# Kernel tuning notes

Hardware: AMD Instinct MI355X
Metric: run time of the kernel (lower is better)

The kernel has to match this reference:

```python
import jax, jax.numpy as jnp
import numpy as np

NUM_HEADS = 12

def setup_inputs() -> dict:
    key = jax.random.key(0)
    k1, k2, k3 = jax.random.split(key, 3)
    B, N, C = 8, 2048, 768
    x = jax.random.normal(k1, (B, N, C), dtype=jnp.float32)
    w_qkv = jax.random.normal(k2, (3 * C, C), dtype=jnp.float32) * (C ** -0.5)
    w_proj = jax.random.normal(k3, (C, C), dtype=jnp.float32) * (C ** -0.5)
    b_proj = jnp.zeros((C,), dtype=jnp.float32)
    return {"x": x, "w_qkv": w_qkv, "w_proj": w_proj, "b_proj": b_proj}

def reference(x, w_qkv, w_proj, b_proj):
    B, N, C = x.shape
    H = NUM_HEADS
    D = C // H
    scale = D ** -0.5
    # qkv: [B,N,3C] -> [3,B,H,N,D]
    qkv = (x @ w_qkv.T).reshape(B, N, 3, H, D).transpose(2, 0, 3, 1, 4)
    q, k, v = qkv[0], qkv[1], qkv[2]
    attn = jnp.einsum('bhnd,bhmd->bhnm', q, k) * scale  # [B,H,N,N]
    attn = jax.nn.softmax(attn, axis=-1)
    out = jnp.einsum('bhnm,bhmd->bhnd', attn, v)  # [B,H,N,D]
    out = out.transpose(0, 2, 1, 3).reshape(B, N, C)
    return out @ w_proj.T + b_proj
```

## Files before the change

### kernel.cpp

```cpp
#include <hip/hip_runtime.h>

typedef __bf16 bf16;
typedef __attribute__((ext_vector_type(8))) __bf16 bf16x8;
typedef __attribute__((ext_vector_type(4))) __bf16 bf16x4;
typedef __attribute__((ext_vector_type(4))) float f32x4;

#define NBATCH 8
#define NHEAD  12
#define SEQ    2048
#define DH     64
#define CDIM   768
#define MROWS  (NBATCH*SEQ)
#define NQKV   (3*CDIM)

__device__ __forceinline__ f32x4 mfma16(bf16x8 a, bf16x8 b, f32x4 c) {
  return __builtin_amdgcn_mfma_f32_16x16x32_bf16(a, b, c, 0, 0, 0);
}

__device__ __forceinline__ void gload_lds16(const void* g, void* l) {
  __builtin_amdgcn_global_load_lds((const __attribute__((address_space(1))) void*)g,
                                   (__attribute__((address_space(3))) void*)l,
                                   16, 0, 0);
}

__device__ __forceinline__ unsigned cvt_pk_bf16(float lo, float hi) {
  unsigned r;
  asm("v_cvt_pk_bf16_f32 %0, %1, %2" : "=v"(r) : "v"(lo), "v"(hi));
  return r;
}

__device__ __forceinline__ float exp2_raw(float x) {
  float r;
  asm("v_exp_f32 %0, %1" : "=v"(r) : "v"(x));
  return r;
}

__global__ void cvt_bf16(const float* __restrict__ src, bf16* __restrict__ dst, int n8) {
  int i = blockIdx.x * 256 + threadIdx.x;
  if (i >= n8) return;
  const float4* s4 = (const float4*)src;
  float4 a = s4[2*i], c = s4[2*i+1];
  bf16x8 o;
  o[0]=(bf16)a.x; o[1]=(bf16)a.y; o[2]=(bf16)a.z; o[3]=(bf16)a.w;
  o[4]=(bf16)c.x; o[5]=(bf16)c.y; o[6]=(bf16)c.z; o[7]=(bf16)c.w;
  *(bf16x8*)(dst + (size_t)i*8) = o;
}

template <int OUT_F32>
__global__ __launch_bounds__(256, 2)
void gemm_bt(const bf16* __restrict__ A, const bf16* __restrict__ Bm,
             void* __restrict__ Cout, const float* __restrict__ bias,
             int M, int Nn, int K) {
  __shared__ bf16 As[128*32];
  __shared__ bf16 Bs[128*32];
  const int tid = threadIdx.x, wid = tid >> 6, lane = tid & 63;
  const int g = lane >> 4, ln = lane & 15;
  const int ntn = Nn >> 7;
  const int gsz = 32 * ntn;
  const int grp = blockIdx.x / gsz;
  const int rem = blockIdx.x - grp * gsz;
  const int tm = grp * 32 + (rem & 31);
  const int tn = rem >> 5;
  const int m0 = tm << 7, n0 = tn << 7;
  const int wr = wid >> 1, wc = wid & 1;

  const int srow = lane >> 2;
  const int sslot = lane & 3;

  f32x4 acc[4][4] = {};

  const int nkt = K >> 5;
  for (int kt = 0; kt < nkt; ++kt) {
    if (kt) __syncthreads();
    #pragma unroll
    for (int i = 0; i < 2; ++i) {
      int c = wid * 2 + i;
      int row = c * 16 + srow;
      int colA = kt * 32 + ((sslot ^ (row & 3)) << 3);
      gload_lds16(A + (size_t)(m0 + row) * K + colA, &As[c * 512]);
      gload_lds16(Bm + (size_t)(n0 + row) * K + colA, &Bs[c * 512]);
    }
    __syncthreads();

    bf16x8 aF[4], bF[4];
    #pragma unroll
    for (int m = 0; m < 4; ++m) {
      int row = wr * 64 + m * 16 + ln;
      aF[m] = *(const bf16x8*)&As[row * 32 + ((g ^ (row & 3)) << 3)];
    }
    #pragma unroll
    for (int n = 0; n < 4; ++n) {
      int row = wc * 64 + n * 16 + ln;
      bF[n] = *(const bf16x8*)&Bs[row * 32 + ((g ^ (row & 3)) << 3)];
    }
    #pragma unroll
    for (int m = 0; m < 4; ++m)
      #pragma unroll
      for (int n = 0; n < 4; ++n)
        acc[m][n] = mfma16(aF[m], bF[n], acc[m][n]);
  }

  #pragma unroll
  for (int m = 0; m < 4; ++m) {
    int rowb = m0 + wr * 64 + m * 16 + g * 4;
    #pragma unroll
    for (int n = 0; n < 4; ++n) {
      int col = n0 + wc * 64 + n * 16 + ln;
      float bv = OUT_F32 ? bias[col] : 0.f;
      #pragma unroll
      for (int r = 0; r < 4; ++r) {
        if (OUT_F32)
          ((float*)Cout)[(size_t)(rowb + r) * Nn + col] = acc[m][n][r] + bv;
        else
          ((bf16*)Cout)[(size_t)(rowb + r) * Nn + col] = (bf16)acc[m][n][r];
      }
    }
  }
}

__global__ __launch_bounds__(256)
void split_v(const bf16* __restrict__ qkv, bf16* __restrict__ Vt) {
  __shared__ bf16 vlds[64 * 72];
  const int nt = blockIdx.x, bh = blockIdx.y;
  const int b = bh / NHEAD, h = bh % NHEAD;
  const int tid = threadIdx.x;
  const int nl = tid >> 2, quad = tid & 3;

  const bf16* s = qkv + ((size_t)(b * SEQ + nt * 64 + nl)) * NQKV + 2 * CDIM + h * DH + quad * 16;
  *(bf16x8*)&vlds[nl * 72 + quad * 16] = *(const bf16x8*)s;
  *(bf16x8*)&vlds[nl * 72 + quad * 16 + 8] = *(const bf16x8*)(s + 8);
  __syncthreads();
  const int dl = tid >> 2;
  bf16x8 w0, w1;
  #pragma unroll
  for (int j = 0; j < 8; ++j) {
    w0[j] = vlds[(quad * 16 + j) * 72 + dl];
    w1[j] = vlds[(quad * 16 + 8 + j) * 72 + dl];
  }
  bf16* d = Vt + ((size_t)bh * DH + dl) * SEQ + nt * 64 + quad * 16;
  *(bf16x8*)d = w0;
  *(bf16x8*)(d + 8) = w1;
}

__global__ __launch_bounds__(512, 4)
void attn_fwd12(const bf16* __restrict__ qkv, const bf16* __restrict__ Vt,
                bf16* __restrict__ Oa) {
  __shared__ bf16 Ks[2][4096];
  __shared__ bf16 Vs[2][4096];
  const int tid = threadIdx.x, wid = tid >> 6, lane = tid & 63;
  const int g = lane >> 4, ln = lane & 15;
  const int qt = blockIdx.x, bh = blockIdx.y;
  const int b = bh / NHEAD, h = bh % NHEAD;

  const bf16* QrowA = qkv + ((size_t)b * SEQ + qt * 256 + wid * 32 + ln) * NQKV + h * DH;
  const bf16* QrowB = QrowA + (size_t)16 * NQKV;
  const bf16x8 qA0 = *(const bf16x8*)(QrowA + g * 8);
  const bf16x8 qA1 = *(const bf16x8*)(QrowA + 32 + g * 8);
  const bf16x8 qB0 = *(const bf16x8*)(QrowB + g * 8);
  const bf16x8 qB1 = *(const bf16x8*)(QrowB + 32 + g * 8);

  const int sr = lane >> 3, sl = lane & 7;
  const int pr = wid * 8 + sr;
  const int sw = (sl ^ (pr & 7)) << 3;
  const int keyK = ((pr >> 5) & 1) * 32 + ((pr >> 4) & 1) * 4 + ((pr >> 2) & 3) * 8 + (pr & 3);
  const bf16* kp = qkv + ((size_t)b * SEQ + keyK) * NQKV + CDIM + h * DH + sw;
  const bf16* vp = Vt + ((size_t)bh * DH + pr) * SEQ + sw;
  const int lofs = wid * 512;
  const size_t KADV = (size_t)64 * NQKV;

  const int e7 = ln & 7;
  const int off0 = ln * 64 + ((g ^ e7) << 3);
  const int off1 = ln * 64 + (((4 | g) ^ e7) << 3);

  const bf16 one = (bf16)1.0f;
  const bf16x8 onesF = {one, one, one, one, one, one, one, one};

  f32x4 oA[4] = {}, oB[4] = {};
  f32x4 laccA = {0.f, 0.f, 0.f, 0.f}, laccB = {0.f, 0.f, 0.f, 0.f};
  float mA = -3.0e38f, mB = -3.0e38f;
  const float SC = 0.125f * 1.44269504088896f;

  gload_lds16(kp, &Ks[0][lofs]);
  gload_lds16(vp, &Vs[0][lofs]);
  kp += KADV; vp += 64;
  gload_lds16(kp, &Ks[1][lofs]);
  gload_lds16(vp, &Vs[1][lofs]);
  kp += KADV; vp += 64;

  const int NT = SEQ / 64;
  for (int t = 0; t < NT; ++t) {
    if (t == NT - 1) asm volatile("s_waitcnt vmcnt(0)" ::: "memory");
    else             asm volatile("s_waitcnt vmcnt(2)" ::: "memory");
    __builtin_amdgcn_s_barrier();
    __builtin_amdgcn_sched_barrier(0);

    const bf16* KsB = &Ks[t & 1][0];
    const bf16* VsB = &Vs[t & 1][0];

    f32x4 sA[4] = {}, sB[4] = {};
    #pragma unroll
    for (int nt = 0; nt < 4; ++nt) {
      bf16x8 kF0 = *(const bf16x8*)(KsB + off0 + nt * 1024);
      bf16x8 kF1 = *(const bf16x8*)(KsB + off1 + nt * 1024);
      sA[nt] = mfma16(kF0, qA0, sA[nt]);
      sA[nt] = mfma16(kF1, qA1, sA[nt]);
      sB[nt] = mfma16(kF0, qB0, sB[nt]);
      sB[nt] = mfma16(kF1, qB1, sB[nt]);
    }

    float a0 = fmaxf(fmaxf(sA[0][0], sA[0][1]), fmaxf(sA[0][2], sA[0][3]));
    float a1 = fmaxf(fmaxf(sA[1][0], sA[1][1]), fmaxf(sA[1][2], sA[1][3]));
    float a2 = fmaxf(fmaxf(sA[2][0], sA[2][1]), fmaxf(sA[2][2], sA[2][3]));
    float a3 = fmaxf(fmaxf(sA[3][0], sA[3][1]), fmaxf(sA[3][2], sA[3][3]));
    float rA = fmaxf(fmaxf(a0, a1), fmaxf(a2, a3));
    rA = fmaxf(rA, __shfl_xor(rA, 16, 64));
    rA = fmaxf(rA, __shfl_xor(rA, 32, 64));
    float b0 = fmaxf(fmaxf(sB[0][0], sB[0][1]), fmaxf(sB[0][2], sB[0][3]));
    float b1 = fmaxf(fmaxf(sB[1][0], sB[1][1]), fmaxf(sB[1][2], sB[1][3]));
    float b2 = fmaxf(fmaxf(sB[2][0], sB[2][1]), fmaxf(sB[2][2], sB[2][3]));
    float b3 = fmaxf(fmaxf(sB[3][0], sB[3][1]), fmaxf(sB[3][2], sB[3][3]));
    float rB = fmaxf(fmaxf(b0, b1), fmaxf(b2, b3));
    rB = fmaxf(rB, __shfl_xor(rB, 16, 64));
    rB = fmaxf(rB, __shfl_xor(rB, 32, 64));
    const float rsA = rA * SC, rsB = rB * SC;

    if (__any(rsA > mA + 8.0f || rsB > mB + 8.0f)) {
      float nmA = fmaxf(mA, rsA), nmB = fmaxf(mB, rsB);
      float alA = exp2_raw(mA - nmA), alB = exp2_raw(mB - nmB);
      mA = nmA; mB = nmB;
      float alrA[4], alrB[4];
      #pragma unroll
      for (int r = 0; r < 4; ++r) {
        alrA[r] = __shfl(alA, g * 4 + r, 64);
        alrB[r] = __shfl(alB, g * 4 + r, 64);
      }
      #pragma unroll
      for (int dt = 0; dt < 4; ++dt)
        #pragma unroll
        for (int r = 0; r < 4; ++r) { oA[dt][r] *= alrA[r]; oB[dt][r] *= alrB[r]; }
      #pragma unroll
      for (int r = 0; r < 4; ++r) { laccA[r] *= alrA[r]; laccB[r] *= alrB[r]; }
    }

    bf16x8 pA[2], pB[2];
    #pragma unroll
    for (int kk = 0; kk < 2; ++kk) {
      union { bf16x8 v; unsigned u[4]; } w;
      w.u[0] = cvt_pk_bf16(exp2_raw(fmaf(sA[2*kk][0], SC, -mA)),
                           exp2_raw(fmaf(sA[2*kk][1], SC, -mA)));
      w.u[1] = cvt_pk_bf16(exp2_raw(fmaf(sA[2*kk][2], SC, -mA)),
                           exp2_raw(fmaf(sA[2*kk][3], SC, -mA)));
      w.u[2] = cvt_pk_bf16(exp2_raw(fmaf(sA[2*kk+1][0], SC, -mA)),
                           exp2_raw(fmaf(sA[2*kk+1][1], SC, -mA)));
      w.u[3] = cvt_pk_bf16(exp2_raw(fmaf(sA[2*kk+1][2], SC, -mA)),
                           exp2_raw(fmaf(sA[2*kk+1][3], SC, -mA)));
      pA[kk] = w.v;
      w.u[0] = cvt_pk_bf16(exp2_raw(fmaf(sB[2*kk][0], SC, -mB)),
                           exp2_raw(fmaf(sB[2*kk][1], SC, -mB)));
      w.u[1] = cvt_pk_bf16(exp2_raw(fmaf(sB[2*kk][2], SC, -mB)),
                           exp2_raw(fmaf(sB[2*kk][3], SC, -mB)));
      w.u[2] = cvt_pk_bf16(exp2_raw(fmaf(sB[2*kk+1][0], SC, -mB)),
                           exp2_raw(fmaf(sB[2*kk+1][1], SC, -mB)));
      w.u[3] = cvt_pk_bf16(exp2_raw(fmaf(sB[2*kk+1][2], SC, -mB)),
                           exp2_raw(fmaf(sB[2*kk+1][3], SC, -mB)));
      pB[kk] = w.v;
    }

    #pragma unroll
    for (int kk = 0; kk < 2; ++kk) {
      laccA = mfma16(pA[kk], onesF, laccA);
      laccB = mfma16(pB[kk], onesF, laccB);
      const int voff = kk ? off1 : off0;
      #pragma unroll
      for (int dt = 0; dt < 4; ++dt) {
        bf16x8 vF = *(const bf16x8*)(VsB + voff + dt * 1024);
        oA[dt] = mfma16(pA[kk], vF, oA[dt]);
        oB[dt] = mfma16(pB[kk], vF, oB[dt]);
      }
    }

    __builtin_amdgcn_sched_barrier(0);
    __builtin_amdgcn_s_barrier();
    if (t + 2 < NT) {
      gload_lds16(kp, &Ks[t & 1][lofs]);
      gload_lds16(vp, &Vs[t & 1][lofs]);
      kp += KADV; vp += 64;
    }
  }

  float invA[4], invB[4];
  #pragma unroll
  for (int r = 0; r < 4; ++r) { invA[r] = 1.0f / laccA[r]; invB[r] = 1.0f / laccB[r]; }

  #pragma unroll
  for (int r = 0; r < 4; ++r) {
    bf16* OrA = Oa + ((size_t)b * SEQ + qt * 256 + wid * 32 + g * 4 + r) * CDIM + h * DH + ln;
    bf16* OrB = OrA + (size_t)16 * CDIM;
    #pragma unroll
    for (int dt = 0; dt < 4; ++dt) {
      OrA[dt * 16] = (bf16)(oA[dt][r] * invA[r]);
      OrB[dt * 16] = (bf16)(oB[dt][r] * invB[r]);
    }
  }
}

extern "C" void kernel_launch(void* const* d_in, const int* in_sizes, int n_in,
                              void* d_out, int out_size, void* d_ws, size_t ws_size,
                              hipStream_t stream) {
  const float* x      = (const float*)d_in[0];
  const float* w_qkv  = (const float*)d_in[1];
  const float* w_proj = (const float*)d_in[2];
  const float* b_proj = (const float*)d_in[3];

  char* ws = (char*)d_ws;
  bf16* x_bf    = (bf16*)(ws + 0);
  bf16* wqkv_bf = (bf16*)(ws + 25165824);
  bf16* wproj_bf= (bf16*)(ws + 28704768);
  bf16* qkv     = (bf16*)(ws + 29884416);
  bf16* attn_o  = (bf16*)(ws + 105381888);
  bf16* Vtb     = (bf16*)(ws + 130547712);

  cvt_bf16<<<dim3((MROWS*CDIM/8 + 255)/256), 256, 0, stream>>>(x, x_bf, MROWS*CDIM/8);
  cvt_bf16<<<dim3((NQKV*CDIM/8 + 255)/256), 256, 0, stream>>>(w_qkv, wqkv_bf, NQKV*CDIM/8);
  cvt_bf16<<<dim3((CDIM*CDIM/8 + 255)/256), 256, 0, stream>>>(w_proj, wproj_bf, CDIM*CDIM/8);

  gemm_bt<0><<<dim3((MROWS/128)*(NQKV/128)), 256, 0, stream>>>(
      x_bf, wqkv_bf, qkv, nullptr, MROWS, NQKV, CDIM);

  split_v<<<dim3(SEQ/64, NBATCH*NHEAD), 256, 0, stream>>>(qkv, Vtb);

  attn_fwd12<<<dim3(SEQ/256, NBATCH*NHEAD), 512, 0, stream>>>(qkv, Vtb, attn_o);

  gemm_bt<1><<<dim3((MROWS/128)*(CDIM/128)), 256, 0, stream>>>(
      attn_o, wproj_bf, (float*)d_out, b_proj, MROWS, CDIM, CDIM);
}
```

Before: 263.2 us.

## Double-buffer LDS in projection GEMM to overlap global loads with MFMA

Converts the QKV/projection GEMM's single LDS tile into a two-stage double buffer. The next k-tile is prefetched via global_load_lds while the current one is consumed, with manual vmcnt waits and barriers in place of the per-iteration load-then-sync pattern. The intent is to hide global memory latency behind MFMA work. It doubles LDS use (32KB per block), which could affect occupancy at 2 blocks/SM, and relies on hand-placed waitcnt correctness.

```diff
diff --git a/kernel.cpp b/kernel.cpp
--- a/kernel.cpp
+++ b/kernel.cpp
@@ -51,8 +51,8 @@
 void gemm_bt(const bf16* __restrict__ A, const bf16* __restrict__ Bm,
              void* __restrict__ Cout, const float* __restrict__ bias,
              int M, int Nn, int K) {
-  __shared__ bf16 As[128*32];
-  __shared__ bf16 Bs[128*32];
+  __shared__ bf16 As[2][128*32];
+  __shared__ bf16 Bs[2][128*32];
   const int tid = threadIdx.x, wid = tid >> 6, lane = tid & 63;
   const int g = lane >> 4, ln = lane & 15;
   const int ntn = Nn >> 7;
@@ -66,39 +66,59 @@
 
   const int srow = lane >> 2;
   const int sslot = lane & 3;
+  const int c0 = wid * 2, c1 = wid * 2 + 1;
+  const int row0 = c0 * 16 + srow, row1 = c1 * 16 + srow;
+  const int sw0 = (sslot ^ (row0 & 3)) << 3;
+  const int sw1 = (sslot ^ (row1 & 3)) << 3;
+  const bf16* a0 = A + (size_t)(m0 + row0) * K + sw0;
+  const bf16* a1 = A + (size_t)(m0 + row1) * K + sw1;
+  const bf16* b0 = Bm + (size_t)(n0 + row0) * K + sw0;
+  const bf16* b1 = Bm + (size_t)(n0 + row1) * K + sw1;
 
   f32x4 acc[4][4] = {};
-
   const int nkt = K >> 5;
+
+#define GSTAGE(BUF) do {                                          \
+    gload_lds16(a0, &As[BUF][c0 * 512]);                          \
+    gload_lds16(a1, &As[BUF][c1 * 512]);                          \
+    gload_lds16(b0, &Bs[BUF][c0 * 512]);                          \
+    gload_lds16(b1, &Bs[BUF][c1 * 512]);                          \
+    a0 += 32; a1 += 32; b0 += 32; b1 += 32;                       \
+  } while (0)
+
+  GSTAGE(0);
+  GSTAGE(1);
+
   for (int kt = 0; kt < nkt; ++kt) {
-    if (kt) __syncthreads();
-    #pragma unroll
-    for (int i = 0; i < 2; ++i) {
-      int c = wid * 2 + i;
-      int row = c * 16 + srow;
-      int colA = kt * 32 + ((sslot ^ (row & 3)) << 3);
-      gload_lds16(A + (size_t)(m0 + row) * K + colA, &As[c * 512]);
-      gload_lds16(Bm + (size_t)(n0 + row) * K + colA, &Bs[c * 512]);
-    }
-    __syncthreads();
-
+    if (kt < nkt - 1) asm volatile("s_waitcnt vmcnt(4)" ::: "memory");
+    else              asm volatile("s_waitcnt vmcnt(0)" ::: "memory");
+    __builtin_amdgcn_s_barrier();
+    __builtin_amdgcn_sched_barrier(0);
+
+    const bf16* AsB = &As[kt & 1][0];
+    const bf16* BsB = &Bs[kt & 1][0];
     bf16x8 aF[4], bF[4];
     #pragma unroll
     for (int m = 0; m < 4; ++m) {
       int row = wr * 64 + m * 16 + ln;
-      aF[m] = *(const bf16x8*)&As[row * 32 + ((g ^ (row & 3)) << 3)];
+      aF[m] = *(const bf16x8*)&AsB[row * 32 + ((g ^ (row & 3)) << 3)];
     }
     #pragma unroll
     for (int n = 0; n < 4; ++n) {
       int row = wc * 64 + n * 16 + ln;
-      bF[n] = *(const bf16x8*)&Bs[row * 32 + ((g ^ (row & 3)) << 3)];
+      bF[n] = *(const bf16x8*)&BsB[row * 32 + ((g ^ (row & 3)) << 3)];
     }
     #pragma unroll
     for (int m = 0; m < 4; ++m)
       #pragma unroll
       for (int n = 0; n < 4; ++n)
         acc[m][n] = mfma16(aF[m], bF[n], acc[m][n]);
-  }
+
+    __builtin_amdgcn_sched_barrier(0);
+    __builtin_amdgcn_s_barrier();
+    if (kt + 2 < nkt) GSTAGE(kt & 1);
+  }
+#undef GSTAGE
 
   #pragma unroll
   for (int m = 0; m < 4; ++m) {
```

Measured after the change: 263.5 us. No clear change (+0.1%).
